# Kernel optimization log

Hardware: AMD Instinct MI355X
Metric: run time of the kernel (lower is better)

Reference implementation:

```python
import jax, jax.numpy as jnp
import numpy as np

K_SIZE = 5  # neighborhood window

def _extract_patches(x, k):
    # tf.image.extract_patches with stride 1, SAME (zero) padding.
    # x: [B,H,W,C] -> [B,H,W,k*k,C]
    pad = k // 2
    B, H, W, C = x.shape
    xp = jnp.pad(x, ((0, 0), (pad, pad), (pad, pad), (0, 0)))
    # fixed small k*k loop (25 shifted views), stacked along patch axis
    return jnp.stack([xp[:, i:i + H, j:j + W, :]
                      for i in range(k) for j in range(k)], axis=3)

def setup_inputs() -> dict:
    key = jax.random.key(0)
    k1, k2, k3 = jax.random.split(key, 3)
    B, H, W, C, BIN = 2, 256, 256, 32, 32
    return {
        "main": jax.random.normal(k1, (B, H, W, C), dtype=jnp.float32),
        "ref": jax.random.normal(k2, (B, H, W, C), dtype=jnp.float32),
        "ref_value": jax.random.normal(k3, (B, H, W, BIN), dtype=jnp.float32),
    }

def reference(main, ref, ref_value):
    # mode='dot': local-window dot-product attention
    ref_stacked = _extract_patches(ref, K_SIZE)          # [B,H,W,k*k,C]
    attn = jnp.einsum('bhwc,bhwkc->bhwk', main, ref_stacked)
    attn = jax.nn.softmax(attn, axis=-1)                 # [B,H,W,k*k]
    # aggregate_mode='weighted_sum'
    ref_value_stacked = _extract_patches(ref_value, K_SIZE)  # [B,H,W,k*k,bin]
    return jnp.einsum('bhwk,bhwki->bhwi', attn, ref_value_stacked)
```

## Files before the change

kernel.cpp:

```cpp
#include <hip/hip_runtime.h>


typedef float v2f __attribute__((ext_vector_type(2)));

template <int CTRL>
__device__ __forceinline__ float dpp_add(float x)
{
    const int y = __builtin_amdgcn_mov_dpp(__float_as_int(x), CTRL, 0xF, 0xF, true);
    return x + __int_as_float(y);
}

__global__ void __launch_bounds__(256)
local_attn_kernel(const float* __restrict__ main_p,
                  const float* __restrict__ ref_p,
                  const float* __restrict__ rv_p,
                  float* __restrict__ out_p)
{
    const int tid  = threadIdx.x;
    const int lane = tid & 63;
    const int wv   = tid >> 6;
    const int s    = lane & 3;
    const int pw   = lane >> 2;

    const int bid  = blockIdx.x;
    const int ct   = bid & 15;
    const int band = (bid >> 4) & 63;
    const int b    = bid >> 10;

    const int col0 = ct * 16;
    const int hb   = band * 4;
    const int ib   = b << 16;

    const int wcol = col0 + pw;
    const int prow = hb + wv;

    const float4* m4 = (const float4*)main_p;
    const float4* r4 = (const float4*)ref_p;
    const float4* v4 = (const float4*)rv_p;
    float4*       o4 = (float4*)out_p;

    __shared__ float4 smem[2][160];

    const bool stg = (tid < 160);
    int pos0 = 0; const float4* sp0 = r4;
    if (stg) {
        const int col_0 = tid >> 3, u0 = tid & 7;
        pos0 = col_0 * 8 + ((u0 + col_0) & 7);
        const int g0 = min(max(col0 - 2 + col_0, 0), 255);
        sp0 = r4 + (((ib + g0) << 3) + u0);
    }

    float cmask[5];
    int   idxA[5], idxB[5];
    int   vb[5];
#pragma unroll
    for (int j = 0; j < 5; ++j) {
        cmask[j] = ((unsigned)(wcol + j - 2) < 256u) ? 1.0f : 0.0f;
        const int lc = pw + j;
        idxA[j] = lc * 8 + ((2 * s     + lc) & 7);
        idxB[j] = lc * 8 + ((2 * s + 1 + lc) & 7);
        const int gc = min(max(wcol + j - 2, 0), 255);
        vb[j] = ((ib + gc) << 3) + 2 * s;
    }

    const float L2E = 1.44269504088896340736f;

    v2f mA, mB, mC, mD;
    {
        const int pbase = ((ib + prow * 256 + wcol) << 3) + 2 * s;
        const float4 t0 = m4[pbase];
        const float4 t1 = m4[pbase + 1];
        mA = (v2f){t0.x * L2E, t0.y * L2E};
        mB = (v2f){t0.z * L2E, t0.w * L2E};
        mC = (v2f){t1.x * L2E, t1.y * L2E};
        mD = (v2f){t1.z * L2E, t1.w * L2E};
    }
    v2f aA = {0.f, 0.f}, aB = {0.f, 0.f}, aC = {0.f, 0.f}, aD = {0.f, 0.f};
    float sum = 0.0f;

    if (stg) {
        const int roff = (min(max(hb - 2, 0), 255)) << 11;
        smem[0][pos0] = sp0[roff];
    }
    __syncthreads();

#pragma unroll 1
    for (int rr = 0; rr < 8; ++rr) {
        float4 st0;
        const bool more = (rr < 7);
        if (more && stg) {
            const int roff = (min(max(hb + rr - 1, 0), 255)) << 11;
            st0 = sp0[roff];
        }

        if (rr >= wv && rr <= wv + 4) {
            const int   gr    = hb + rr - 2;
            const float rok   = ((unsigned)gr < 256u) ? 1.0f : 0.0f;
            const int   croff = (min(max(gr, 0), 255)) << 11;
            const float4* bp  = &smem[rr & 1][0];

#pragma unroll
            for (int j = 0; j < 5; ++j) {
                const float4 rA4 = bp[idxA[j]];
                const float4 rB4 = bp[idxB[j]];
                const float4 vA4 = v4[vb[j] + croff];
                const float4 vB4 = v4[vb[j] + croff + 1];
                const float  mj  = cmask[j] * rok;

                v2f p = mA * (v2f){rA4.x, rA4.y};
                p = mB * (v2f){rA4.z, rA4.w} + p;
                p = mC * (v2f){rB4.x, rB4.y} + p;
                p = mD * (v2f){rB4.z, rB4.w} + p;
                float sc = p.x + p.y;
                sc = dpp_add<0xB1>(sc);
                sc = dpp_add<0x4E>(sc);

                const float e = __builtin_exp2f(sc * mj);
                sum += e;
                const float t = e * mj;
                const v2f t2 = {t, t};
                aA = t2 * (v2f){vA4.x, vA4.y} + aA;
                aB = t2 * (v2f){vA4.z, vA4.w} + aB;
                aC = t2 * (v2f){vB4.x, vB4.y} + aC;
                aD = t2 * (v2f){vB4.z, vB4.w} + aD;
            }
        }

        if (more) {
            if (stg) smem[(rr + 1) & 1][pos0] = st0;
            __syncthreads();
        }
    }

    const float inv = 1.0f / sum;
    const int obase = ((ib + prow * 256 + wcol) << 3) + 2 * s;
    o4[obase]     = make_float4(aA.x * inv, aA.y * inv, aB.x * inv, aB.y * inv);
    o4[obase + 1] = make_float4(aC.x * inv, aC.y * inv, aD.x * inv, aD.y * inv);
}

extern "C" void kernel_launch(void* const* d_in, const int* in_sizes, int n_in,
                              void* d_out, int out_size, void* d_ws, size_t ws_size,
                              hipStream_t stream)
{
    const float* main_p = (const float*)d_in[0];
    const float* ref_p  = (const float*)d_in[1];
    const float* rv_p   = (const float*)d_in[2];
    float*       out_p  = (float*)d_out;

    const int npix   = in_sizes[0] / 32;
    const int blocks = npix / 64;
    local_attn_kernel<<<blocks, 256, 0, stream>>>(main_p, ref_p, rv_p, out_p);
}
```

Before: 110.5 us.

## Stage ref and ref_value rows in LDS as packed fp16

The kernel now stages ref_value rows in shared memory alongside ref. Before, it read the value vectors straight from global memory for every window tap. Both tensors are converted to packed half precision on the way into LDS. This halves LDS footprint and bandwidth and removes redundant global loads of ref_value across the 5 column taps. The cost is fp16 rounding of the inputs, which loses accuracy and may exceed tolerance, plus extra conversion instructions in the inner loop.

```diff
diff --git a/kernel.cpp b/kernel.cpp
--- a/kernel.cpp
+++ b/kernel.cpp
@@ -1,4 +1,5 @@
 #include <hip/hip_runtime.h>
+#include <hip/hip_fp16.h>
 
 
 typedef float v2f __attribute__((ext_vector_type(2)));
@@ -8,6 +9,25 @@
 {
     const int y = __builtin_amdgcn_mov_dpp(__float_as_int(x), CTRL, 0xF, 0xF, true);
     return x + __int_as_float(y);
+}
+
+__device__ __forceinline__ unsigned pkh(float a, float b)
+{
+    const __half2 h = __float22half2_rn(make_float2(a, b));
+    return __builtin_bit_cast(unsigned, h);
+}
+
+__device__ __forceinline__ v2f uph(unsigned u)
+{
+    const __half2 h = __builtin_bit_cast(__half2, u);
+    const float2 f = __half22float2(h);
+    return (v2f){f.x, f.y};
+}
+
+__device__ __forceinline__ uint4 pack8(const float4 f0, const float4 f1)
+{
+    return make_uint4(pkh(f0.x, f0.y), pkh(f0.z, f0.w),
+                      pkh(f1.x, f1.y), pkh(f1.z, f1.w));
 }
 
 __global__ void __launch_bounds__(256)
@@ -39,29 +59,21 @@
     const float4* v4 = (const float4*)rv_p;
     float4*       o4 = (float4*)out_p;
 
-    __shared__ float4 smem[2][160];
+    __shared__ uint4 sm[2][160];
 
     const bool stg = (tid < 160);
-    int pos0 = 0; const float4* sp0 = r4;
+    const float4* sp = r4;
     if (stg) {
-        const int col_0 = tid >> 3, u0 = tid & 7;
-        pos0 = col_0 * 8 + ((u0 + col_0) & 7);
-        const int g0 = min(max(col0 - 2 + col_0, 0), 255);
-        sp0 = r4 + (((ib + g0) << 3) + u0);
+        const int c  = (tid < 80) ? tid : tid - 80;
+        const int lc = c >> 2, cs = c & 3;
+        const int g  = min(max(col0 - 2 + lc, 0), 255);
+        sp = ((tid < 80) ? r4 : v4) + (((ib + g) << 3) + 2 * cs);
     }
 
     float cmask[5];
-    int   idxA[5], idxB[5];
-    int   vb[5];
 #pragma unroll
-    for (int j = 0; j < 5; ++j) {
+    for (int j = 0; j < 5; ++j)
         cmask[j] = ((unsigned)(wcol + j - 2) < 256u) ? 1.0f : 0.0f;
-        const int lc = pw + j;
-        idxA[j] = lc * 8 + ((2 * s     + lc) & 7);
-        idxB[j] = lc * 8 + ((2 * s + 1 + lc) & 7);
-        const int gc = min(max(wcol + j - 2, 0), 255);
-        vb[j] = ((ib + gc) << 3) + 2 * s;
-    }
 
     const float L2E = 1.44269504088896340736f;
 
@@ -80,37 +92,35 @@
 
     if (stg) {
         const int roff = (min(max(hb - 2, 0), 255)) << 11;
-        smem[0][pos0] = sp0[roff];
+        sm[0][tid] = pack8(sp[roff], sp[roff + 1]);
     }
     __syncthreads();
 
 #pragma unroll 1
     for (int rr = 0; rr < 8; ++rr) {
-        float4 st0;
+        float4 f0, f1;
         const bool more = (rr < 7);
         if (more && stg) {
             const int roff = (min(max(hb + rr - 1, 0), 255)) << 11;
-            st0 = sp0[roff];
+            f0 = sp[roff];
+            f1 = sp[roff + 1];
         }
 
         if (rr >= wv && rr <= wv + 4) {
-            const int   gr    = hb + rr - 2;
-            const float rok   = ((unsigned)gr < 256u) ? 1.0f : 0.0f;
-            const int   croff = (min(max(gr, 0), 255)) << 11;
-            const float4* bp  = &smem[rr & 1][0];
+            const int   gr  = hb + rr - 2;
+            const float rok = ((unsigned)gr < 256u) ? 1.0f : 0.0f;
+            const uint4* bp = &sm[rr & 1][0];
 
 #pragma unroll
             for (int j = 0; j < 5; ++j) {
-                const float4 rA4 = bp[idxA[j]];
-                const float4 rB4 = bp[idxB[j]];
-                const float4 vA4 = v4[vb[j] + croff];
-                const float4 vB4 = v4[vb[j] + croff + 1];
-                const float  mj  = cmask[j] * rok;
+                const uint4 uR = bp[lane + 4 * j];
+                const uint4 uV = bp[80 + lane + 4 * j];
+                const float mj = cmask[j] * rok;
 
-                v2f p = mA * (v2f){rA4.x, rA4.y};
-                p = mB * (v2f){rA4.z, rA4.w} + p;
-                p = mC * (v2f){rB4.x, rB4.y} + p;
-                p = mD * (v2f){rB4.z, rB4.w} + p;
+                v2f p = mA * uph(uR.x);
+                p = mB * uph(uR.y) + p;
+                p = mC * uph(uR.z) + p;
+                p = mD * uph(uR.w) + p;
                 float sc = p.x + p.y;
                 sc = dpp_add<0xB1>(sc);
                 sc = dpp_add<0x4E>(sc);
@@ -119,15 +129,15 @@
                 sum += e;
                 const float t = e * mj;
                 const v2f t2 = {t, t};
-                aA = t2 * (v2f){vA4.x, vA4.y} + aA;
-                aB = t2 * (v2f){vA4.z, vA4.w} + aB;
-                aC = t2 * (v2f){vB4.x, vB4.y} + aC;
-                aD = t2 * (v2f){vB4.z, vB4.w} + aD;
+                aA = t2 * uph(uV.x) + aA;
+                aB = t2 * uph(uV.y) + aB;
+                aC = t2 * uph(uV.z) + aC;
+                aD = t2 * uph(uV.w) + aD;
             }
         }
 
         if (more) {
-            if (stg) smem[(rr + 1) & 1][pos0] = st0;
+            if (stg) sm[(rr + 1) & 1][tid] = pack8(f0, f1);
             __syncthreads();
         }
     }
```

Result: faster. 102.6 us (-7.1%).
